# Optimization experiments

Measured on AMD Instinct MI355X. Metric: run time of the kernel, lower is better.

## Reference

```python
import jax, jax.numpy as jnp
import numpy as np

KERNEL = 3
STRIDE = 1
PADDING = 1
DILATION = 1
GRID_SIZE = 3
SPLINE_ORDER = 2
IN_CH = 3
OUT_CH = 32
IN_FEAT = IN_CH * KERNEL * KERNEL  # 27
N_BASIS = GRID_SIZE + SPLINE_ORDER  # 5


def _make_grid():
    # efficient-kan grid: uniform knots over [-1, 1] extended by spline_order on each side
    h = 2.0 / GRID_SIZE
    g = np.arange(-SPLINE_ORDER, GRID_SIZE + SPLINE_ORDER + 1, dtype=np.float32) * h - 1.0
    return jnp.asarray(np.broadcast_to(g, (IN_FEAT, g.shape[0])))  # (27, 8)


def b_splines(x, grid):
    # x: (N, F); grid: (F, G). Cox-de Boor recursion.
    x = x[:, :, None]                      # (N, F, 1)
    g = grid[None, :, :]                   # (1, F, G)
    bases = ((x >= g[..., :-1]) & (x < g[..., 1:])).astype(x.dtype)
    for k in range(1, SPLINE_ORDER + 1):
        bases = ((x - g[..., : -(k + 1)]) / (g[..., k:-1] - g[..., : -(k + 1)]) * bases[..., :-1]
                 + (g[..., k + 1:] - x) / (g[..., k + 1:] - g[..., 1:-k]) * bases[..., 1:])
    return bases  # (N, F, N_BASIS)


def setup_inputs() -> dict:
    key = jax.random.key(0)
    k1, k2, k3, k4 = jax.random.split(key, 4)
    x = jax.random.normal(k1, (16, IN_CH, 256, 256), dtype=jnp.float32)
    # Kaiming-ish init scales (values irrelevant for correctness testing)
    base_weight = jax.random.normal(k2, (OUT_CH, IN_FEAT), dtype=jnp.float32) * (1.0 / np.sqrt(IN_FEAT))
    spline_weight = jax.random.normal(k3, (OUT_CH, IN_FEAT, N_BASIS), dtype=jnp.float32) * 0.1
    spline_scaler = jax.random.normal(k4, (OUT_CH, IN_FEAT), dtype=jnp.float32) * (1.0 / np.sqrt(IN_FEAT))
    grid = _make_grid()
    return {"x": x, "base_weight": base_weight, "spline_weight": spline_weight,
            "spline_scaler": spline_scaler, "grid": grid}


def reference(x, base_weight, spline_weight, spline_scaler, grid):
    B, C, H, W = x.shape
    out_h = (H + 2 * PADDING - DILATION * (KERNEL - 1) - 1) // STRIDE + 1
    out_w = (W + 2 * PADDING - DILATION * (KERNEL - 1) - 1) // STRIDE + 1
    # im2col: (B, C*k*k, out_h, out_w), feature ordering (C, kh, kw) matches torch Unfold
    patches = jax.lax.conv_general_dilated_patches(
        x, filter_shape=(KERNEL, KERNEL), window_strides=(STRIDE, STRIDE),
        padding=((PADDING, PADDING), (PADDING, PADDING)), rhs_dilation=(DILATION, DILATION))
    pf = patches.reshape(B, IN_FEAT, out_h * out_w).transpose(0, 2, 1).reshape(-1, IN_FEAT)  # (N, 27)
    # KANLinear: silu base branch + scaled spline branch
    base = jnp.einsum('nf,of->no', jax.nn.silu(pf), base_weight)
    bases = b_splines(pf, grid)                                   # (N, 27, 5)
    scaled_sw = spline_weight * spline_scaler[:, :, None]         # (O, 27, 5)
    spline = jnp.einsum('nfk,ofk->no', bases, scaled_sw)
    out = base + spline                                           # (N, O)
    return out.reshape(B, out_h * out_w, OUT_CH).transpose(0, 2, 1).reshape(B, OUT_CH, out_h, out_w)
```

## Files before the change

### kernel.cpp

```cpp
#include <hip/hip_runtime.h>

#define IN_CH 3
#define OUT_CH 32
#define IN_FEAT 27
#define NB 5
#define NG 8
#define HH 256
#define WW 256
#define NPIX (16 * HH * WW)

#define RECE 24
#define RECP 28
#define TW 66
#define TROWS 10
#define NREC (TROWS * TW)
#define WB_HALVES (9 * 2 * 64 * 8)
#define WS_NEEDED ((size_t)WB_HALVES * 2 + 16)

typedef __attribute__((ext_vector_type(8))) _Float16 half8;
typedef __attribute__((ext_vector_type(4))) float f32x4;
typedef __attribute__((ext_vector_type(4))) unsigned int u32x4;

__device__ inline void kan_phi6(float xx, const float* g, const float* r1, const float* r2,
                                float* o6) {
    const float sig = 1.0f / (1.0f + __expf(-xx));
    o6[0] = xx * sig;
    float b0[7];
#pragma unroll
    for (int j = 0; j < 7; ++j) b0[j] = (xx >= g[j] && xx < g[j + 1]) ? 1.0f : 0.0f;
    float b1[6];
#pragma unroll
    for (int j = 0; j < 6; ++j)
        b1[j] = (xx - g[j]) * r1[j] * b0[j] + (g[j + 2] - xx) * r1[j + 1] * b0[j + 1];
#pragma unroll
    for (int j = 0; j < NB; ++j)
        o6[1 + j] = (xx - g[j]) * r2[j] * b1[j] + (g[j + 3] - xx) * r2[j + 1] * b1[j + 1];
}

__device__ inline void load_grid(const float* __restrict__ grid, float* g, float* r1, float* r2) {
#pragma unroll
    for (int j = 0; j < NG; ++j) g[j] = grid[j];
#pragma unroll
    for (int j = 0; j < NG - 1; ++j) r1[j] = 1.0f / (g[j + 1] - g[j]);
#pragma unroll
    for (int j = 0; j < NG - 2; ++j) r2[j] = 1.0f / (g[j + 2] - g[j]);
}

__global__ void kan_prepW(const float* __restrict__ bw, const float* __restrict__ sw,
                          const float* __restrict__ ss, const float* __restrict__ grid,
                          _Float16* __restrict__ wb) {
    int t = blockIdx.x * 256 + threadIdx.x;
    if (t >= 9 * 2 * 64) return;

    if (t == 0) {
        float* gt = (float*)(wb + WB_HALVES);
        gt[0] = grid[0];
        gt[1] = 7.0f / (grid[7] - grid[0]);
    }

    const int lane = t & 63;
    const int nt = (t >> 6) & 1;
    const int tap = t >> 7;
    const int o = nt * 16 + (lane & 15);
    const int kbase = (lane >> 4) * 8;
    half8 v8 = {0, 0, 0, 0, 0, 0, 0, 0};
#pragma unroll
    for (int e = 0; e < 8; ++e) {
        int kk = kbase + e;
        float v = 0.0f;
        if (kk < 18) {
            int c = kk / 6, j = kk % 6;
            int f = c * 9 + tap;
            int of = o * IN_FEAT + f;
            v = (j == 0) ? bw[of] : sw[of * NB + (j - 1)] * ss[of];
        }
        v8[e] = (_Float16)v;
    }
    *(half8*)(wb + (size_t)t * 8) = v8;
}

__global__ __launch_bounds__(256) void kan_fused(const float* __restrict__ x,
                                                 const _Float16* __restrict__ wb,
                                                 float* __restrict__ out) {
    __shared__ _Float16 lPhi[NREC * RECP];

    const int tid = threadIdx.x;
    const int bid = blockIdx.x;
    const int strip = bid & 3;
    const int rowg = (bid >> 2) & 31;
    const int b = bid >> 7;
    const int h0 = rowg * 8;
    const int w0 = strip * 64;

    const int lane = tid & 63;
    const int wid = tid >> 6;
    const int r = lane & 15;
    const int gq = lane >> 4;

    half8 bf[18];
#pragma unroll
    for (int i = 0; i < 18; ++i)
        bf[i] = *(const half8*)(wb + ((size_t)(i * 64 + lane)) * 8);

    const float* gt = (const float*)(wb + WB_HALVES);
    const float g0 = gt[0];
    const float invh = gt[1];

    for (int ri = tid; ri < NREC; ri += 256) {
        const int dyR = ri / TW;
        const int wxR = ri - dyR * TW - 1;
        const int hy = h0 + dyR - 1;
        const int wx = w0 + wxR;
        const bool vld = ((unsigned)hy < HH) & ((unsigned)wx < WW);

        _Float16 rec[RECE];
#pragma unroll
        for (int c = 0; c < IN_CH; ++c) {
            const float xx = vld ? x[((b * IN_CH + c) << 16) + (hy << 8) + wx] : 0.0f;
            const float sig = 1.0f / (1.0f + __expf(-xx));
            rec[c * 6] = (_Float16)(xx * sig);
            const float u = (xx - g0) * invh;
            const float fi = floorf(u);
            const int i0 = (int)fi;
            const float t = u - fi;
            const float om = 1.0f - t;
            float wA = 0.5f * om * om;
            float wC = 0.5f * t * t;
            float wB = 1.0f - wA - wC;
            const bool valid = (fi >= 0.0f) & (i0 <= 6);
            wA = valid ? wA : 0.0f;
            wB = valid ? wB : 0.0f;
            wC = valid ? wC : 0.0f;
#pragma unroll
            for (int j = 0; j < NB; ++j) {
                float v = (j == i0 - 2) ? wA : ((j == i0 - 1) ? wB : ((j == i0) ? wC : 0.0f));
                rec[c * 6 + 1 + j] = (_Float16)v;
            }
        }
#pragma unroll
        for (int j = 18; j < RECE; ++j) rec[j] = (_Float16)0.0f;

        half8* dst = (half8*)(lPhi + ri * RECP);
        dst[0] = *(half8*)(rec + 0);
        dst[1] = *(half8*)(rec + 8);
        dst[2] = *(half8*)(rec + 16);
    }
    __syncthreads();

    const int row0 = wid * 2;
    const int hr0 = h0 + row0;
#pragma unroll
    for (int m = 0; m < 4; ++m) {
        half8 haf[4][3];
#pragma unroll
        for (int hr = 0; hr < 4; ++hr) {
#pragma unroll
            for (int dx = 0; dx < 3; ++dx) {
                const int ridx = (row0 + hr) * TW + m * 16 + r + dx;
                half8 v = {0, 0, 0, 0, 0, 0, 0, 0};
                if (gq < 3) v = *(const half8*)(lPhi + ridx * RECP + gq * 8);
                haf[hr][dx] = v;
            }
        }

        f32x4 a00 = {0.f, 0.f, 0.f, 0.f};
        f32x4 a01 = {0.f, 0.f, 0.f, 0.f};
        f32x4 a10 = {0.f, 0.f, 0.f, 0.f};
        f32x4 a11 = {0.f, 0.f, 0.f, 0.f};
#pragma unroll
        for (int dy = 0; dy < 3; ++dy) {
#pragma unroll
            for (int dx = 0; dx < 3; ++dx) {
                const int tap = dy * 3 + dx;
                a00 = __builtin_amdgcn_mfma_f32_16x16x32_f16(haf[dy][dx],     bf[tap * 2 + 0], a00, 0, 0, 0);
                a01 = __builtin_amdgcn_mfma_f32_16x16x32_f16(haf[dy][dx],     bf[tap * 2 + 1], a01, 0, 0, 0);
                a10 = __builtin_amdgcn_mfma_f32_16x16x32_f16(haf[dy + 1][dx], bf[tap * 2 + 0], a10, 0, 0, 0);
                a11 = __builtin_amdgcn_mfma_f32_16x16x32_f16(haf[dy + 1][dx], bf[tap * 2 + 1], a11, 0, 0, 0);
            }
        }

        const int wcol = w0 + m * 16 + gq * 4;
        float* p00 = out + ((size_t)(b * OUT_CH + r) << 16)      + (hr0 << 8)       + wcol;
        float* p01 = out + ((size_t)(b * OUT_CH + 16 + r) << 16) + (hr0 << 8)       + wcol;
        float* p10 = out + ((size_t)(b * OUT_CH + r) << 16)      + ((hr0 + 1) << 8) + wcol;
        float* p11 = out + ((size_t)(b * OUT_CH + 16 + r) << 16) + ((hr0 + 1) << 8) + wcol;
        *(f32x4*)p00 = a00;
        *(f32x4*)p01 = a01;
        *(f32x4*)p10 = a10;
        *(f32x4*)p11 = a11;
    }
}

__global__ void kan_combine_weights(const float* __restrict__ bw,
                                    const float* __restrict__ sw,
                                    const float* __restrict__ ss,
                                    float* __restrict__ wc) {
    int idx = blockIdx.x * blockDim.x + threadIdx.x;
    if (idx >= IN_FEAT * 6 * OUT_CH) return;
    int o = idx & 31;
    int j = (idx >> 5) % 6;
    int f = idx / (6 * 32);
    float v;
    if (j == 0) v = bw[o * IN_FEAT + f];
    else        v = sw[(o * IN_FEAT + f) * NB + (j - 1)] * ss[o * IN_FEAT + f];
    wc[idx] = v;
}

__global__ __launch_bounds__(256) void kan_main(const float* __restrict__ x,
                                                const float* __restrict__ grid,
                                                const float* __restrict__ wc,
                                                float* __restrict__ out) {
    const int p = blockIdx.x * blockDim.x + threadIdx.x;
    const int w = p & (WW - 1);
    const int h = (p >> 8) & (HH - 1);
    const int b = p >> 16;
    float g[NG], r1[NG - 1], r2[NG - 2];
    load_grid(grid, g, r1, r2);
    float acc[OUT_CH];
#pragma unroll
    for (int o = 0; o < OUT_CH; ++o) acc[o] = 0.0f;
    const float* xb = x + b * (IN_CH * HH * WW);
    for (int c = 0; c < IN_CH; ++c) {
        const float* xc = xb + c * (HH * WW);
#pragma unroll
        for (int dy = 0; dy < 3; ++dy) {
            const int hy = h + dy - 1;
            const bool vy = (hy >= 0) && (hy < HH);
#pragma unroll
            for (int dx = 0; dx < 3; ++dx) {
                const int wx = w + dx - 1;
                const bool vld = vy && (wx >= 0) && (wx < WW);
                const float xx = vld ? xc[hy * WW + wx] : 0.0f;
                float o6[6];
                kan_phi6(xx, g, r1, r2, o6);
                const float* wf = wc + (c * 9 + dy * 3 + dx) * (6 * OUT_CH);
#pragma unroll
                for (int jj = 0; jj < 6; ++jj) {
                    const float* wj = wf + jj * OUT_CH;
#pragma unroll
                    for (int o = 0; o < OUT_CH; ++o) acc[o] += o6[jj] * wj[o];
                }
            }
        }
    }
    float* ob = out + (size_t)b * (OUT_CH * HH * WW) + h * WW + w;
#pragma unroll
    for (int o = 0; o < OUT_CH; ++o) ob[o * (HH * WW)] = acc[o];
}

extern "C" void kernel_launch(void* const* d_in, const int* in_sizes, int n_in,
                              void* d_out, int out_size, void* d_ws, size_t ws_size,
                              hipStream_t stream) {
    const float* x    = (const float*)d_in[0];
    const float* bw   = (const float*)d_in[1];
    const float* sw   = (const float*)d_in[2];
    const float* ss   = (const float*)d_in[3];
    const float* grid = (const float*)d_in[4];
    float* out = (float*)d_out;

    if (ws_size >= WS_NEEDED) {
        _Float16* wb = (_Float16*)d_ws;
        kan_prepW<<<(9 * 2 * 64 + 255) / 256, 256, 0, stream>>>(bw, sw, ss, grid, wb);
        kan_fused<<<NPIX / 512, 256, 0, stream>>>(x, wb, out);
    } else {
        float* wc = (float*)d_ws;
        kan_combine_weights<<<(IN_FEAT * 6 * OUT_CH + 255) / 256, 256, 0, stream>>>(bw, sw, ss, wc);
        kan_main<<<NPIX / 256, 256, 0, stream>>>(x, grid, wc, out);
    }
}
```

Before: 49.69 us.

## Make fused KAN conv blocks persistent over row bands with double-buffered LDS

Each block now covers a 32-row by 64-column band in 8 tiles of 4 rows instead of a single 8-row tile, which cuts the grid to 512 blocks. Phi tiles are double-buffered in LDS: the global loads for the next tile are issued before the MFMA work on the current one, and the conversion into the other buffer happens after it. Halo recomputation per output row drops from 10/8 to 6/4, weight fragments are loaded once per block, and launch_bounds asks for 2 blocks per CU. The cost is fewer blocks, which may leave CUs underfilled, plus more register pressure.

```diff
diff --git a/kernel.cpp b/kernel.cpp
--- a/kernel.cpp
+++ b/kernel.cpp
@@ -12,14 +12,14 @@
 #define RECE 24
 #define RECP 28
 #define TW 66
-#define TROWS 10
+#define TROWS 6
 #define NREC (TROWS * TW)
+#define NTILES 8
 #define WB_HALVES (9 * 2 * 64 * 8)
 #define WS_NEEDED ((size_t)WB_HALVES * 2 + 16)
 
 typedef __attribute__((ext_vector_type(8))) _Float16 half8;
 typedef __attribute__((ext_vector_type(4))) float f32x4;
-typedef __attribute__((ext_vector_type(4))) unsigned int u32x4;
 
 __device__ inline void kan_phi6(float xx, const float* g, const float* r1, const float* r2,
                                 float* o6) {
@@ -79,17 +79,17 @@
     *(half8*)(wb + (size_t)t * 8) = v8;
 }
 
-__global__ __launch_bounds__(256) void kan_fused(const float* __restrict__ x,
-                                                 const _Float16* __restrict__ wb,
-                                                 float* __restrict__ out) {
-    __shared__ _Float16 lPhi[NREC * RECP];
+__global__ __launch_bounds__(256, 2) void kan_fused(const float* __restrict__ x,
+                                                    const _Float16* __restrict__ wb,
+                                                    float* __restrict__ out) {
+    __shared__ _Float16 lPhi[2][NREC * RECP];
 
     const int tid = threadIdx.x;
     const int bid = blockIdx.x;
     const int strip = bid & 3;
-    const int rowg = (bid >> 2) & 31;
-    const int b = bid >> 7;
-    const int h0 = rowg * 8;
+    const int hband = (bid >> 2) & 7;
+    const int b = bid >> 5;
+    const int h0 = hband * 32;
     const int w0 = strip * 64;
 
     const int lane = tid & 63;
@@ -106,88 +106,109 @@
     const float g0 = gt[0];
     const float invh = gt[1];
 
-    for (int ri = tid; ri < NREC; ri += 256) {
-        const int dyR = ri / TW;
-        const int wxR = ri - dyR * TW - 1;
-        const int hy = h0 + dyR - 1;
-        const int wx = w0 + wxR;
-        const bool vld = ((unsigned)hy < HH) & ((unsigned)wx < WW);
-
-        _Float16 rec[RECE];
+    const int ri0 = tid;
+    const int ri1 = tid + 256;
+    const int dy0 = ri0 / TW, wx0r = ri0 - dy0 * TW - 1;
+    const int dy1 = ri1 / TW, wx1r = ri1 - dy1 * TW - 1;
+    const int wx0 = w0 + wx0r, wx1 = w0 + wx1r;
+    const bool cOK0 = ((unsigned)wx0 < WW);
+    const bool cOK1 = (ri1 < NREC) && ((unsigned)wx1 < WW);
+
+    float xr0[IN_CH], xr1[IN_CH];
+
+    auto issue_loads = [&](int t) {
+        const int hbase = h0 + t * 4 - 1;
+        const int hy0 = hbase + dy0;
+        const int hy1 = hbase + dy1;
+        const bool v0 = cOK0 & ((unsigned)hy0 < HH);
+        const bool v1 = cOK1 & ((unsigned)hy1 < HH);
 #pragma unroll
         for (int c = 0; c < IN_CH; ++c) {
-            const float xx = vld ? x[((b * IN_CH + c) << 16) + (hy << 8) + wx] : 0.0f;
-            const float sig = 1.0f / (1.0f + __expf(-xx));
-            rec[c * 6] = (_Float16)(xx * sig);
-            const float u = (xx - g0) * invh;
-            const float fi = floorf(u);
-            const int i0 = (int)fi;
-            const float t = u - fi;
-            const float om = 1.0f - t;
-            float wA = 0.5f * om * om;
-            float wC = 0.5f * t * t;
-            float wB = 1.0f - wA - wC;
-            const bool valid = (fi >= 0.0f) & (i0 <= 6);
-            wA = valid ? wA : 0.0f;
-            wB = valid ? wB : 0.0f;
-            wC = valid ? wC : 0.0f;
-#pragma unroll
-            for (int j = 0; j < NB; ++j) {
-                float v = (j == i0 - 2) ? wA : ((j == i0 - 1) ? wB : ((j == i0) ? wC : 0.0f));
-                rec[c * 6 + 1 + j] = (_Float16)v;
-            }
-        }
-#pragma unroll
-        for (int j = 18; j < RECE; ++j) rec[j] = (_Float16)0.0f;
-
-        half8* dst = (half8*)(lPhi + ri * RECP);
-        dst[0] = *(half8*)(rec + 0);
-        dst[1] = *(half8*)(rec + 8);
-        dst[2] = *(half8*)(rec + 16);
-    }
+            xr0[c] = v0 ? x[((b * IN_CH + c) << 16) + (hy0 << 8) + wx0] : 0.0f;
+            xr1[c] = v1 ? x[((b * IN_CH + c) << 16) + (hy1 << 8) + wx1] : 0.0f;
+        }
+    };
+
+    auto convert = [&](int buf) {
+        _Float16* dstb = lPhi[buf];
+#pragma unroll
+        for (int k = 0; k < 2; ++k) {
+            const int ri = k ? ri1 : ri0;
+            if (k && ri1 >= NREC) break;
+            const float* xr = k ? xr1 : xr0;
+            _Float16 rec[RECE];
+#pragma unroll
+            for (int c = 0; c < IN_CH; ++c) {
+                const float xx = xr[c];
+                const float sig = 1.0f / (1.0f + __expf(-xx));
+                rec[c * 6] = (_Float16)(xx * sig);
+                const float u = (xx - g0) * invh;
+                const float fi = floorf(u);
+                const int i0 = (int)fi;
+                const float t = u - fi;
+                const float om = 1.0f - t;
+                float wA = 0.5f * om * om;
+                float wC = 0.5f * t * t;
+                float wB = 1.0f - wA - wC;
+                const bool valid = (fi >= 0.0f) & (i0 <= 6);
+                wA = valid ? wA : 0.0f;
+                wB = valid ? wB : 0.0f;
+                wC = valid ? wC : 0.0f;
+#pragma unroll
+                for (int j = 0; j < NB; ++j) {
+                    float v = (j == i0 - 2) ? wA : ((j == i0 - 1) ? wB : ((j == i0) ? wC : 0.0f));
+                    rec[c * 6 + 1 + j] = (_Float16)v;
+                }
+            }
+#pragma unroll
+            for (int j = 18; j < RECE; ++j) rec[j] = (_Float16)0.0f;
+            half8* dst = (half8*)(dstb + ri * RECP);
+            dst[0] = *(half8*)(rec + 0);
+            dst[1] = *(half8*)(rec + 8);
+            dst[2] = *(half8*)(rec + 16);
+        }
+    };
+
+    issue_loads(0);
+    convert(0);
     __syncthreads();
 
-    const int row0 = wid * 2;
-    const int hr0 = h0 + row0;
-#pragma unroll
-    for (int m = 0; m < 4; ++m) {
-        half8 haf[4][3];
-#pragma unroll
-        for (int hr = 0; hr < 4; ++hr) {
-#pragma unroll
-            for (int dx = 0; dx < 3; ++dx) {
-                const int ridx = (row0 + hr) * TW + m * 16 + r + dx;
-                half8 v = {0, 0, 0, 0, 0, 0, 0, 0};
-                if (gq < 3) v = *(const half8*)(lPhi + ridx * RECP + gq * 8);
-                haf[hr][dx] = v;
-            }
-        }
-
-        f32x4 a00 = {0.f, 0.f, 0.f, 0.f};
-        f32x4 a01 = {0.f, 0.f, 0.f, 0.f};
-        f32x4 a10 = {0.f, 0.f, 0.f, 0.f};
-        f32x4 a11 = {0.f, 0.f, 0.f, 0.f};
-#pragma unroll
-        for (int dy = 0; dy < 3; ++dy) {
-#pragma unroll
-            for (int dx = 0; dx < 3; ++dx) {
-                const int tap = dy * 3 + dx;
-                a00 = __builtin_amdgcn_mfma_f32_16x16x32_f16(haf[dy][dx],     bf[tap * 2 + 0], a00, 0, 0, 0);
-                a01 = __builtin_amdgcn_mfma_f32_16x16x32_f16(haf[dy][dx],     bf[tap * 2 + 1], a01, 0, 0, 0);
-                a10 = __builtin_amdgcn_mfma_f32_16x16x32_f16(haf[dy + 1][dx], bf[tap * 2 + 0], a10, 0, 0, 0);
-                a11 = __builtin_amdgcn_mfma_f32_16x16x32_f16(haf[dy + 1][dx], bf[tap * 2 + 1], a11, 0, 0, 0);
-            }
-        }
-
-        const int wcol = w0 + m * 16 + gq * 4;
-        float* p00 = out + ((size_t)(b * OUT_CH + r) << 16)      + (hr0 << 8)       + wcol;
-        float* p01 = out + ((size_t)(b * OUT_CH + 16 + r) << 16) + (hr0 << 8)       + wcol;
-        float* p10 = out + ((size_t)(b * OUT_CH + r) << 16)      + ((hr0 + 1) << 8) + wcol;
-        float* p11 = out + ((size_t)(b * OUT_CH + 16 + r) << 16) + ((hr0 + 1) << 8) + wcol;
-        *(f32x4*)p00 = a00;
-        *(f32x4*)p01 = a01;
-        *(f32x4*)p10 = a10;
-        *(f32x4*)p11 = a11;
+    int cur = 0;
+    for (int t = 0; t < NTILES; ++t) {
+        const bool more = (t + 1 < NTILES);
+        if (more) issue_loads(t + 1);
+
+        const _Float16* lp = lPhi[cur];
+        const int hrow = h0 + t * 4 + wid;
+        float* pb0 = out + ((size_t)(b * OUT_CH + r) << 16)      + (hrow << 8) + w0 + gq * 4;
+        float* pb1 = out + ((size_t)(b * OUT_CH + 16 + r) << 16) + (hrow << 8) + w0 + gq * 4;
+#pragma unroll
+        for (int m = 0; m < 4; ++m) {
+            half8 af[9];
+#pragma unroll
+            for (int dy = 0; dy < 3; ++dy) {
+#pragma unroll
+                for (int dx = 0; dx < 3; ++dx) {
+                    const int ridx = (wid + dy) * TW + m * 16 + r + dx;
+                    half8 v = {0, 0, 0, 0, 0, 0, 0, 0};
+                    if (gq < 3) v = *(const half8*)(lp + ridx * RECP + gq * 8);
+                    af[dy * 3 + dx] = v;
+                }
+            }
+            f32x4 acc0 = {0.f, 0.f, 0.f, 0.f};
+            f32x4 acc1 = {0.f, 0.f, 0.f, 0.f};
+#pragma unroll
+            for (int tap = 0; tap < 9; ++tap) {
+                acc0 = __builtin_amdgcn_mfma_f32_16x16x32_f16(af[tap], bf[tap * 2 + 0], acc0, 0, 0, 0);
+                acc1 = __builtin_amdgcn_mfma_f32_16x16x32_f16(af[tap], bf[tap * 2 + 1], acc1, 0, 0, 0);
+            }
+            *(f32x4*)(pb0 + m * 16) = acc0;
+            *(f32x4*)(pb1 + m * 16) = acc1;
+        }
+
+        if (more) convert(cur ^ 1);
+        __syncthreads();
+        cur ^= 1;
     }
 }
 
@@ -261,7 +282,7 @@
     if (ws_size >= WS_NEEDED) {
         _Float16* wb = (_Float16*)d_ws;
         kan_prepW<<<(9 * 2 * 64 + 255) / 256, 256, 0, stream>>>(bw, sw, ss, grid, wb);
-        kan_fused<<<NPIX / 512, 256, 0, stream>>>(x, wb, out);
+        kan_fused<<<NPIX / (64 * 32), 256, 0, stream>>>(x, wb, out);
     } else {
         float* wc = (float*)d_ws;
         kan_combine_weights<<<(IN_FEAT * 6 * OUT_CH + 255) / 256, 256, 0, stream>>>(bw, sw, ss, wc);
```

Measured after the change: 74.05 us. +49.0%, slower.

## Shrink fused tile to one output row per wave and use nontemporal stores

Applied to the files above, without the earlier changes.

Halves the per-block output tile from 8 rows to 4 rows, so each wave computes one row instead of two. The LDS halo tile shrinks from 10 to 6 rows and the grid doubles. This trades more halo recomputation of phi records (6/4 vs 10/8 rows) for more blocks, smaller LDS and fewer registers, which should raise occupancy. Output stores become nontemporal so the large output stream does not pollute the cache.

```diff
diff --git a/kernel.cpp b/kernel.cpp
--- a/kernel.cpp
+++ b/kernel.cpp
@@ -12,14 +12,13 @@
 #define RECE 24
 #define RECP 28
 #define TW 66
-#define TROWS 10
+#define TROWS 6
 #define NREC (TROWS * TW)
 #define WB_HALVES (9 * 2 * 64 * 8)
 #define WS_NEEDED ((size_t)WB_HALVES * 2 + 16)
 
 typedef __attribute__((ext_vector_type(8))) _Float16 half8;
 typedef __attribute__((ext_vector_type(4))) float f32x4;
-typedef __attribute__((ext_vector_type(4))) unsigned int u32x4;
 
 __device__ inline void kan_phi6(float xx, const float* g, const float* r1, const float* r2,
                                 float* o6) {
@@ -87,9 +86,9 @@
     const int tid = threadIdx.x;
     const int bid = blockIdx.x;
     const int strip = bid & 3;
-    const int rowg = (bid >> 2) & 31;
-    const int b = bid >> 7;
-    const int h0 = rowg * 8;
+    const int rowg = (bid >> 2) & 63;
+    const int b = bid >> 8;
+    const int h0 = rowg * 4;
     const int w0 = strip * 64;
 
     const int lane = tid & 63;
@@ -147,47 +146,33 @@
     }
     __syncthreads();
 
-    const int row0 = wid * 2;
-    const int hr0 = h0 + row0;
+    const int hrow = h0 + wid;
+    float* pb0 = out + ((size_t)(b * OUT_CH + r) << 16)      + (hrow << 8) + w0 + gq * 4;
+    float* pb1 = out + ((size_t)(b * OUT_CH + 16 + r) << 16) + (hrow << 8) + w0 + gq * 4;
 #pragma unroll
     for (int m = 0; m < 4; ++m) {
-        half8 haf[4][3];
-#pragma unroll
-        for (int hr = 0; hr < 4; ++hr) {
+        half8 af[9];
+#pragma unroll
+        for (int dy = 0; dy < 3; ++dy) {
 #pragma unroll
             for (int dx = 0; dx < 3; ++dx) {
-                const int ridx = (row0 + hr) * TW + m * 16 + r + dx;
+                const int ridx = (wid + dy) * TW + m * 16 + r + dx;
                 half8 v = {0, 0, 0, 0, 0, 0, 0, 0};
                 if (gq < 3) v = *(const half8*)(lPhi + ridx * RECP + gq * 8);
-                haf[hr][dx] = v;
+                af[dy * 3 + dx] = v;
             }
         }
 
-        f32x4 a00 = {0.f, 0.f, 0.f, 0.f};
-        f32x4 a01 = {0.f, 0.f, 0.f, 0.f};
-        f32x4 a10 = {0.f, 0.f, 0.f, 0.f};
-        f32x4 a11 = {0.f, 0.f, 0.f, 0.f};
-#pragma unroll
-        for (int dy = 0; dy < 3; ++dy) {
-#pragma unroll
-            for (int dx = 0; dx < 3; ++dx) {
-                const int tap = dy * 3 + dx;
-                a00 = __builtin_amdgcn_mfma_f32_16x16x32_f16(haf[dy][dx],     bf[tap * 2 + 0], a00, 0, 0, 0);
-                a01 = __builtin_amdgcn_mfma_f32_16x16x32_f16(haf[dy][dx],     bf[tap * 2 + 1], a01, 0, 0, 0);
-                a10 = __builtin_amdgcn_mfma_f32_16x16x32_f16(haf[dy + 1][dx], bf[tap * 2 + 0], a10, 0, 0, 0);
-                a11 = __builtin_amdgcn_mfma_f32_16x16x32_f16(haf[dy + 1][dx], bf[tap * 2 + 1], a11, 0, 0, 0);
-            }
-        }
-
-        const int wcol = w0 + m * 16 + gq * 4;
-        float* p00 = out + ((size_t)(b * OUT_CH + r) << 16)      + (hr0 << 8)       + wcol;
-        float* p01 = out + ((size_t)(b * OUT_CH + 16 + r) << 16) + (hr0 << 8)       + wcol;
-        float* p10 = out + ((size_t)(b * OUT_CH + r) << 16)      + ((hr0 + 1) << 8) + wcol;
-        float* p11 = out + ((size_t)(b * OUT_CH + 16 + r) << 16) + ((hr0 + 1) << 8) + wcol;
-        *(f32x4*)p00 = a00;
-        *(f32x4*)p01 = a01;
-        *(f32x4*)p10 = a10;
-        *(f32x4*)p11 = a11;
+        f32x4 acc0 = {0.f, 0.f, 0.f, 0.f};
+        f32x4 acc1 = {0.f, 0.f, 0.f, 0.f};
+#pragma unroll
+        for (int tap = 0; tap < 9; ++tap) {
+            acc0 = __builtin_amdgcn_mfma_f32_16x16x32_f16(af[tap], bf[tap * 2 + 0], acc0, 0, 0, 0);
+            acc1 = __builtin_amdgcn_mfma_f32_16x16x32_f16(af[tap], bf[tap * 2 + 1], acc1, 0, 0, 0);
+        }
+
+        __builtin_nontemporal_store(acc0, (f32x4*)(pb0 + m * 16));
+        __builtin_nontemporal_store(acc1, (f32x4*)(pb1 + m * 16));
     }
 }
 
@@ -261,7 +246,7 @@
     if (ws_size >= WS_NEEDED) {
         _Float16* wb = (_Float16*)d_ws;
         kan_prepW<<<(9 * 2 * 64 + 255) / 256, 256, 0, stream>>>(bw, sw, ss, grid, wb);
-        kan_fused<<<NPIX / 512, 256, 0, stream>>>(x, wb, out);
+        kan_fused<<<NPIX / 256, 256, 0, stream>>>(x, wb, out);
     } else {
         float* wc = (float*)d_ws;
         kan_combine_weights<<<(IN_FEAT * 6 * OUT_CH + 255) / 256, 256, 0, stream>>>(bw, sw, ss, wc);
```

New measurement: 56.64 us. 1.14x slower.
